# Kernel tuning notes

Measured on AMD Instinct MI355X. Metric: run time of the kernel, lower is better.

Reference implementation:

```python
import jax, jax.numpy as jnp
import numpy as np

S = 1024      # MAX_SEQ_LEN
D_IN = 4096
H = 32        # num_heads
G = 8         # num_kv_groups
HD = 128      # head_dim
GS = H // G   # group_size


def _rope(t, cos, sin):
    # t: [heads, S, HD]; cos/sin: [S, HD]
    half = HD // 2
    t1, t2 = t[..., :half], t[..., half:]
    rotated = jnp.concatenate([-t2, t1], axis=-1)
    return t * cos[None] + rotated * sin[None]


def setup_inputs() -> dict:
    key = jax.random.key(0)
    ks = jax.random.split(key, 8)
    x = jax.random.normal(ks[0], (1, S, D_IN), dtype=jnp.float32)
    mask = jnp.triu(jnp.ones((S, S), dtype=bool), k=1)  # causal: True above diagonal
    # RoPE tables (standard llama frequencies)
    inv_freq = 1.0 / (10000.0 ** (jnp.arange(0, HD, 2, dtype=jnp.float32) / HD))
    angles = jnp.arange(S, dtype=jnp.float32)[:, None] * inv_freq[None, :]  # [S, HD/2]
    angles = jnp.concatenate([angles, angles], axis=-1)                     # [S, HD]
    cos, sin = jnp.cos(angles), jnp.sin(angles)
    sc = 0.02
    Wq = jax.random.normal(ks[1], (D_IN, H * HD), dtype=jnp.float32) * sc
    Wk = jax.random.normal(ks[2], (D_IN, G * HD), dtype=jnp.float32) * sc
    Wv = jax.random.normal(ks[3], (D_IN, G * HD), dtype=jnp.float32) * sc
    Wo = jax.random.normal(ks[4], (H * HD, D_IN), dtype=jnp.float32) * sc
    return {"x": x, "mask": mask, "cos": cos, "sin": sin,
            "Wq": Wq, "Wk": Wk, "Wv": Wv, "Wo": Wo}


def reference(x, mask, cos, sin, Wq, Wk, Wv, Wo):
    b, n_tok, _ = x.shape  # b == 1 (module squeezes dim 0)
    xs = x[0]                                        # [S, d_in]
    q = (xs @ Wq).reshape(n_tok, H, HD).transpose(1, 0, 2)   # [H, S, HD]
    k = (xs @ Wk).reshape(n_tok, G, HD).transpose(1, 0, 2)   # [G, S, HD]
    v = (xs @ Wv).reshape(n_tok, G, HD).transpose(1, 0, 2)   # [G, S, HD]
    q = _rope(q, cos, sin)
    k = _rope(k, cos, sin)
    # GQA expansion: repeat_interleave over head dim
    k = jnp.repeat(k, GS, axis=0)                    # [H, S, HD]
    v = jnp.repeat(v, GS, axis=0)
    scores = jnp.einsum('hsd,htd->hst', q, k)        # [H, S, S]
    scores = jnp.where(mask[None], -jnp.inf, scores) / jnp.sqrt(jnp.float32(HD))
    weights = jax.nn.softmax(scores, axis=-1)
    ctx = jnp.einsum('hst,htd->hsd', weights, v)     # [H, S, HD]
    ctx = ctx.transpose(1, 0, 2).reshape(n_tok, H * HD)
    out = ctx @ Wo                                   # [S, d_in]
    return out[None]                                 # [1, S, d_in]
```

## Files before the change

### kernel.cpp

```cpp
#include <hip/hip_runtime.h>
#include <hip/hip_bf16.h>

#define S_LEN 1024
#define DIN 4096
#define NH 32
#define NG 8
#define HD 128

typedef __bf16 bf16x8 __attribute__((ext_vector_type(8)));
typedef __bf16 bf16x4 __attribute__((ext_vector_type(4)));
typedef float f32x4 __attribute__((ext_vector_type(4)));

__device__ __forceinline__ void gload_lds16(const void* g, void* l) {
  __builtin_amdgcn_global_load_lds(
      (const __attribute__((address_space(1))) unsigned int*)g,
      (__attribute__((address_space(3))) unsigned int*)l, 16, 0, 0);
}

__device__ __forceinline__ unsigned pack2bf(float a, float b) {
  union { __bf16 h[2]; unsigned u; } x;
  x.h[0] = (__bf16)a; x.h[1] = (__bf16)b;
  return x.u;
}

__global__ __launch_bounds__(256) void k_cast(const float* __restrict__ in,
                                              __bf16* __restrict__ out, int n4) {
  int i = blockIdx.x * 256 + threadIdx.x;
  if (i >= n4) return;
  const float4 v = ((const float4*)in)[i];
  bf16x4 o;
  o.x = (__bf16)v.x; o.y = (__bf16)v.y; o.z = (__bf16)v.z; o.w = (__bf16)v.w;
  ((bf16x4*)out)[i] = o;
}

__global__ __launch_bounds__(256) void k_rope(__bf16* __restrict__ Q, __bf16* __restrict__ Kb,
                                              const float* __restrict__ cosT,
                                              const float* __restrict__ sinT) {
  int idx = blockIdx.x * 256 + threadIdx.x;
  int d = (idx & 15) * 4;
  int row = idx >> 4;
  __bf16* p; int s;
  if (row < S_LEN * NH) { p = Q + (size_t)row * HD; s = row >> 5; }
  else { int r = row - S_LEN * NH; p = Kb + (size_t)r * HD; s = r >> 3; }
  const float4 c = *(const float4*)&cosT[s * HD + d];
  const float4 sn = *(const float4*)&sinT[s * HD + d];
  bf16x4 a = *(const bf16x4*)&p[d];
  bf16x4 b = *(const bf16x4*)&p[d + 64];
  bf16x4 oa, ob;
  oa.x = (__bf16)((float)a.x * c.x - (float)b.x * sn.x);
  oa.y = (__bf16)((float)a.y * c.y - (float)b.y * sn.y);
  oa.z = (__bf16)((float)a.z * c.z - (float)b.z * sn.z);
  oa.w = (__bf16)((float)a.w * c.w - (float)b.w * sn.w);
  ob.x = (__bf16)((float)b.x * c.x + (float)a.x * sn.x);
  ob.y = (__bf16)((float)b.y * c.y + (float)a.y * sn.y);
  ob.z = (__bf16)((float)b.z * c.z + (float)a.z * sn.z);
  ob.w = (__bf16)((float)b.w * c.w + (float)a.w * sn.w);
  *(bf16x4*)&p[d] = oa;
  *(bf16x4*)&p[d + 64] = ob;
}

template <int MODE>
__global__ __launch_bounds__(256, 3) void k_gemm(const __bf16* __restrict__ A,
                                                 const float* __restrict__ W0,
                                                 const float* __restrict__ W1,
                                                 const float* __restrict__ W2,
                                                 float* __restrict__ C,
                                                 __bf16* __restrict__ Qb,
                                                 __bf16* __restrict__ Kb,
                                                 __bf16* __restrict__ Vt) {
  __shared__ __bf16 As[2][128 * 64];
  __shared__ unsigned Bp[2][32 * 64];
  const int bm = blockIdx.y, bn = blockIdx.x;
  const int K = DIN, NT = K / 64;

  const float* Wsrc; int ldb, nloc;
  if (MODE == 0) { Wsrc = W0; ldb = 4096; nloc = bn * 64; }
  else {
    if (bn < 64)      { Wsrc = W0; ldb = 4096; nloc = bn * 64; }
    else if (bn < 80) { Wsrc = W1; ldb = 1024; nloc = (bn - 64) * 64; }
    else              { Wsrc = W2; ldb = 1024; nloc = (bn - 80) * 64; }
  }

  const int tid = threadIdx.x, w = tid >> 6;
  const int l = tid & 63, l15 = l & 15, g4 = l >> 4;

  const __bf16* Asrc = A + (size_t)(bm * 128) * K;

  f32x4 acc[2][4];
#pragma unroll
  for (int i = 0; i < 2; ++i)
#pragma unroll
    for (int j = 0; j < 4; ++j)
#pragma unroll
      for (int r = 0; r < 4; ++r) acc[i][j][r] = 0.f;

  float4 breg[2][2];
  const int kp_s[2] = {tid >> 4, 16 + (tid >> 4)};
  const int nn_s = (tid & 15) * 4;

  auto loadB = [&](int t) {
#pragma unroll
    for (int p = 0; p < 2; ++p) {
      const float* src = Wsrc + (size_t)(t * 64 + 2 * kp_s[p]) * ldb + nloc + nn_s;
      breg[p][0] = *(const float4*)src;
      breg[p][1] = *(const float4*)(src + ldb);
    }
  };
  auto writeB = [&](unsigned* dst) {
#pragma unroll
    for (int p = 0; p < 2; ++p) {
      int kp = kp_s[p];
      int cphys = (nn_s >> 2) ^ (kp & 7);
      uint4 d;
      d.x = pack2bf(breg[p][0].x, breg[p][1].x);
      d.y = pack2bf(breg[p][0].y, breg[p][1].y);
      d.z = pack2bf(breg[p][0].z, breg[p][1].z);
      d.w = pack2bf(breg[p][0].w, breg[p][1].w);
      *(uint4*)&dst[kp * 64 + cphys * 4] = d;
    }
  };
  auto issueA = [&](int t, __bf16* dst) {
#pragma unroll
    for (int p = 0; p < 4; ++p) {
      int c = p * 256 + tid;
      int row = c >> 3, gc = (c & 7) ^ (row & 7);
      gload_lds16(Asrc + (size_t)row * K + t * 64 + gc * 8, dst + (p * 256 + w * 64) * 8);
    }
  };
  auto compute = [&](const __bf16* Ab, const unsigned* Bp_) {
    bf16x8 af[2][2];
#pragma unroll
    for (int i = 0; i < 2; ++i) {
      int m = w * 32 + i * 16 + l15;
#pragma unroll
      for (int kk = 0; kk < 2; ++kk)
        af[i][kk] = *(const bf16x8*)((const char*)Ab + m * 128 + (((kk * 4 + g4) ^ (m & 7)) << 4));
    }
    unsigned fbu[2][4][4];
#pragma unroll
    for (int kk = 0; kk < 2; ++kk)
#pragma unroll
      for (int j = 0; j < 4; ++j) {
        int n = j * 16 + l15;
#pragma unroll
        for (int d = 0; d < 4; ++d) {
          int kp = kk * 16 + g4 * 4 + d;
          fbu[kk][j][d] = Bp_[kp * 64 + (((n >> 2) ^ (kp & 7)) << 2) + (n & 3)];
        }
      }
#pragma unroll
    for (int kk = 0; kk < 2; ++kk)
#pragma unroll
      for (int j = 0; j < 4; ++j) {
        union { unsigned u[4]; bf16x8 v; } fb;
        fb.u[0] = fbu[kk][j][0]; fb.u[1] = fbu[kk][j][1];
        fb.u[2] = fbu[kk][j][2]; fb.u[3] = fbu[kk][j][3];
#pragma unroll
        for (int i = 0; i < 2; ++i)
          acc[i][j] = __builtin_amdgcn_mfma_f32_16x16x32_bf16(af[i][kk], fb.v, acc[i][j], 0, 0, 0);
      }
  };

  loadB(0);
  issueA(0, As[0]);
  writeB(Bp[0]);
  __syncthreads();

  for (int t = 0; t < NT; t += 2) {
    loadB(t + 1);
    issueA(t + 1, As[1]);
    compute(As[0], Bp[0]);
    writeB(Bp[1]);
    __syncthreads();
    if (t + 2 < NT) {
      loadB(t + 2);
      issueA(t + 2, As[0]);
    }
    compute(As[1], Bp[1]);
    if (t + 2 < NT) writeB(Bp[0]);
    __syncthreads();
  }

  if constexpr (MODE == 0) {
#pragma unroll
    for (int i = 0; i < 2; ++i)
#pragma unroll
      for (int j = 0; j < 4; ++j)
#pragma unroll
        for (int r = 0; r < 4; ++r) {
          size_t row = bm * 128 + w * 32 + i * 16 + g4 * 4 + r;
          size_t col = bn * 64 + j * 16 + l15;
          C[row * 4096 + col] = acc[i][j][r];
        }
  } else {
    if (bn < 80) {
      __bf16* dst = (bn < 64) ? Qb : Kb;
      int ldc = (bn < 64) ? 4096 : 1024;
#pragma unroll
      for (int i = 0; i < 2; ++i)
#pragma unroll
        for (int j = 0; j < 4; ++j)
#pragma unroll
          for (int r = 0; r < 4; ++r) {
            size_t row = bm * 128 + w * 32 + i * 16 + g4 * 4 + r;
            size_t col = (size_t)nloc + j * 16 + l15;
            dst[row * ldc + col] = (__bf16)acc[i][j][r];
          }
    } else {
#pragma unroll
      for (int i = 0; i < 2; ++i)
#pragma unroll
        for (int j = 0; j < 4; ++j) {
          size_t n = (size_t)nloc + j * 16 + l15;
          size_t m0 = bm * 128 + w * 32 + i * 16 + g4 * 4;
          bf16x4 v;
          v.x = (__bf16)acc[i][j][0]; v.y = (__bf16)acc[i][j][1];
          v.z = (__bf16)acc[i][j][2]; v.w = (__bf16)acc[i][j][3];
          *(bf16x4*)&Vt[n * 1024 + m0] = v;
        }
    }
  }
}

__global__ __launch_bounds__(256) void k_attn(const __bf16* __restrict__ Q,
                                              const __bf16* __restrict__ Kb,
                                              const __bf16* __restrict__ Vt,
                                              __bf16* __restrict__ ctx) {
  __shared__ __align__(16) char lds_raw[65536];
  __bf16* Ks = (__bf16*)lds_raw;
  __bf16* Vs = (__bf16*)(lds_raw + 32768);

  const int h = blockIdx.y, g = h >> 2;
  const int q0 = blockIdx.x * 64;
  const int tid = threadIdx.x, w = tid >> 6, l = tid & 63;
  const int l15 = l & 15, g4 = l >> 4;
  const float scale = 0.08838834764831845f;

  bf16x8 qf[4];
  const int qrow = q0 + w * 16 + l15;
#pragma unroll
  for (int ks = 0; ks < 4; ++ks)
    qf[ks] = *(const bf16x8*)&Q[(size_t)qrow * (NH * HD) + h * HD + ks * 32 + g4 * 8];

  f32x4 acc[8];
#pragma unroll
  for (int i = 0; i < 8; ++i)
#pragma unroll
    for (int r = 0; r < 4; ++r) acc[i][r] = 0.f;
  float m_run = -__builtin_inff(), l_run = 0.f;

  const int ntiles = (q0 + 64 + 127) >> 7;
  for (int kt = 0; kt < ntiles; ++kt) {
    const int kv0 = kt * 128;
#pragma unroll
    for (int p = 0; p < 8; ++p) {
      int c = p * 256 + tid;
      int row = c >> 4, cc = c & 15;
      gload_lds16(&Kb[(size_t)(kv0 + row) * (NG * HD) + g * HD + ((cc ^ (row & 7)) << 3)],
                  &Ks[(p * 256 + w * 64) * 8]);
      gload_lds16(&Vt[(size_t)(g * HD + row) * S_LEN + kv0 + ((cc ^ (row & 7)) << 3)],
                  &Vs[(p * 256 + w * 64) * 8]);
    }
    __syncthreads();

    float sreg[8][4];
    const bool need_mask = (kv0 + 127 > q0);
#pragma unroll
    for (int tf = 0; tf < 8; ++tf) {
      f32x4 sa;
#pragma unroll
      for (int r = 0; r < 4; ++r) sa[r] = 0.f;
      int t_loc = tf * 16 + l15;
#pragma unroll
      for (int ks = 0; ks < 4; ++ks) {
        bf16x8 kf = *(const bf16x8*)((const char*)Ks + t_loc * 256 + (((ks * 4 + g4) ^ (t_loc & 7)) << 4));
        sa = __builtin_amdgcn_mfma_f32_16x16x32_bf16(kf, qf[ks], sa, 0, 0, 0);
      }
#pragma unroll
      for (int r = 0; r < 4; ++r) {
        float v = sa[r] * scale;
        if (need_mask && (kv0 + tf * 16 + g4 * 4 + r) > qrow) v = -__builtin_inff();
        sreg[tf][r] = v;
      }
    }
    float mx = -__builtin_inff();
#pragma unroll
    for (int tf = 0; tf < 8; ++tf)
#pragma unroll
      for (int r = 0; r < 4; ++r) mx = fmaxf(mx, sreg[tf][r]);
    mx = fmaxf(mx, __shfl_xor(mx, 16));
    mx = fmaxf(mx, __shfl_xor(mx, 32));
    const float m_new = fmaxf(m_run, mx);
    const float alpha = __expf(m_run - m_new);
    float ssum = 0.f;
#pragma unroll
    for (int tf = 0; tf < 8; ++tf)
#pragma unroll
      for (int r = 0; r < 4; ++r) {
        sreg[tf][r] = __expf(sreg[tf][r] - m_new);
        ssum += sreg[tf][r];
      }
    ssum += __shfl_xor(ssum, 16);
    ssum += __shfl_xor(ssum, 32);
    l_run = l_run * alpha + ssum;
    m_run = m_new;
    float ar[4];
#pragma unroll
    for (int r = 0; r < 4; ++r) ar[r] = __shfl(alpha, g4 * 4 + r);
#pragma unroll
    for (int nf = 0; nf < 8; ++nf)
#pragma unroll
      for (int r = 0; r < 4; ++r) acc[nf][r] *= ar[r];

    __syncthreads();

    char* pb = lds_raw + w * 4096;
#pragma unroll
    for (int tf = 0; tf < 8; ++tf) {
      int chunkc = 2 * tf + (g4 >> 1);
      int addr = l15 * 256 + ((chunkc ^ (l15 & 7)) << 4) + ((g4 & 1) << 3);
      *(unsigned*)(pb + addr)     = pack2bf(sreg[tf][0], sreg[tf][1]);
      *(unsigned*)(pb + addr + 4) = pack2bf(sreg[tf][2], sreg[tf][3]);
    }
    asm volatile("s_waitcnt lgkmcnt(0)" ::: "memory");
    bf16x8 pf[4];
#pragma unroll
    for (int ks = 0; ks < 4; ++ks)
      pf[ks] = *(const bf16x8*)(pb + l15 * 256 + (((ks * 4 + g4) ^ (l15 & 7)) << 4));
#pragma unroll
    for (int nf = 0; nf < 8; ++nf) {
      int d_loc = nf * 16 + l15;
#pragma unroll
      for (int ks = 0; ks < 4; ++ks) {
        bf16x8 vf = *(const bf16x8*)((const char*)Vs + d_loc * 256 + (((ks * 4 + g4) ^ (d_loc & 7)) << 4));
        acc[nf] = __builtin_amdgcn_mfma_f32_16x16x32_bf16(pf[ks], vf, acc[nf], 0, 0, 0);
      }
    }
    __syncthreads();
  }
  float li[4];
#pragma unroll
  for (int r = 0; r < 4; ++r) li[r] = 1.f / __shfl(l_run, g4 * 4 + r);
#pragma unroll
  for (int nf = 0; nf < 8; ++nf)
#pragma unroll
    for (int r = 0; r < 4; ++r) {
      size_t row = q0 + w * 16 + g4 * 4 + r;
      size_t col = (size_t)h * HD + nf * 16 + l15;
      ctx[row * (NH * HD) + col] = (__bf16)(acc[nf][r] * li[r]);
    }
}

extern "C" void kernel_launch(void* const* d_in, const int* in_sizes, int n_in,
                              void* d_out, int out_size, void* d_ws, size_t ws_size,
                              hipStream_t stream) {
  const float* x    = (const float*)d_in[0];
  const float* cosT = (const float*)d_in[2];
  const float* sinT = (const float*)d_in[3];
  const float* Wq   = (const float*)d_in[4];
  const float* Wk   = (const float*)d_in[5];
  const float* Wv   = (const float*)d_in[6];
  const float* Wo   = (const float*)d_in[7];
  float* out = (float*)d_out;

  char* ws = (char*)d_ws;
  const size_t MB = 1u << 20;
  __bf16* xb   = (__bf16*)(ws + 0);
  __bf16* Qb   = (__bf16*)(ws + 8 * MB);
  __bf16* Kbuf = (__bf16*)(ws + 16 * MB);
  __bf16* Vtb  = (__bf16*)(ws + 18 * MB);
  __bf16* ctxb = (__bf16*)(ws + 0);

  k_cast<<<4096, 256, 0, stream>>>(x, xb, (S_LEN * DIN) / 4);

  k_gemm<1><<<dim3(96, 8), 256, 0, stream>>>(xb, Wq, Wk, Wv, nullptr, Qb, Kbuf, Vtb);

  k_rope<<<2560, 256, 0, stream>>>(Qb, Kbuf, cosT, sinT);

  k_attn<<<dim3(16, 32), 256, 0, stream>>>(Qb, Kbuf, Vtb, ctxb);

  k_gemm<0><<<dim3(64, 8), 256, 0, stream>>>(ctxb, Wo, nullptr, nullptr, out,
                                             nullptr, nullptr, nullptr);
}
```

Baseline: 201.0 us.

## Enlarge GEMM block tile to 128x128 with 2x2 warp layout

Doubles the N dimension of each GEMM block tile from 64 to 128 and arranges the four warps as a 2x2 grid, each computing a 64x64 sub-tile with 16 MFMA accumulators. This raises the compute per LDS fragment load and halves repeated reads of the activation matrix. In exchange it halves the grid sizes, increases register pressure (launch bounds lowered to 2 blocks per CU), and may leave CUs underutilized with fewer waves.

```diff
diff --git a/kernel.cpp b/kernel.cpp
--- a/kernel.cpp
+++ b/kernel.cpp
@@ -60,7 +60,7 @@
 }
 
 template <int MODE>
-__global__ __launch_bounds__(256, 3) void k_gemm(const __bf16* __restrict__ A,
+__global__ __launch_bounds__(256, 2) void k_gemm(const __bf16* __restrict__ A,
                                                  const float* __restrict__ W0,
                                                  const float* __restrict__ W1,
                                                  const float* __restrict__ W2,
@@ -69,54 +69,56 @@
                                                  __bf16* __restrict__ Kb,
                                                  __bf16* __restrict__ Vt) {
   __shared__ __bf16 As[2][128 * 64];
-  __shared__ unsigned Bp[2][32 * 64];
+  __shared__ unsigned Bp[2][32 * 128];
   const int bm = blockIdx.y, bn = blockIdx.x;
   const int K = DIN, NT = K / 64;
 
   const float* Wsrc; int ldb, nloc;
-  if (MODE == 0) { Wsrc = W0; ldb = 4096; nloc = bn * 64; }
+  if (MODE == 0) { Wsrc = W0; ldb = 4096; nloc = bn * 128; }
   else {
-    if (bn < 64)      { Wsrc = W0; ldb = 4096; nloc = bn * 64; }
-    else if (bn < 80) { Wsrc = W1; ldb = 1024; nloc = (bn - 64) * 64; }
-    else              { Wsrc = W2; ldb = 1024; nloc = (bn - 80) * 64; }
+    if (bn < 32)      { Wsrc = W0; ldb = 4096; nloc = bn * 128; }
+    else if (bn < 40) { Wsrc = W1; ldb = 1024; nloc = (bn - 32) * 128; }
+    else              { Wsrc = W2; ldb = 1024; nloc = (bn - 40) * 128; }
   }
 
   const int tid = threadIdx.x, w = tid >> 6;
+  const int wm = w >> 1, wn = w & 1;
   const int l = tid & 63, l15 = l & 15, g4 = l >> 4;
 
   const __bf16* Asrc = A + (size_t)(bm * 128) * K;
 
-  f32x4 acc[2][4];
-#pragma unroll
-  for (int i = 0; i < 2; ++i)
+  f32x4 acc[4][4];
+#pragma unroll
+  for (int i = 0; i < 4; ++i)
 #pragma unroll
     for (int j = 0; j < 4; ++j)
 #pragma unroll
       for (int r = 0; r < 4; ++r) acc[i][j][r] = 0.f;
 
-  float4 breg[2][2];
-  const int kp_s[2] = {tid >> 4, 16 + (tid >> 4)};
-  const int nn_s = (tid & 15) * 4;
+  float4 breg[4][2];
+  const int kp_base = tid >> 5;
+  const int cg = tid & 31;
 
   auto loadB = [&](int t) {
 #pragma unroll
-    for (int p = 0; p < 2; ++p) {
-      const float* src = Wsrc + (size_t)(t * 64 + 2 * kp_s[p]) * ldb + nloc + nn_s;
+    for (int p = 0; p < 4; ++p) {
+      int kp = p * 8 + kp_base;
+      const float* src = Wsrc + (size_t)(t * 64 + 2 * kp) * ldb + nloc + cg * 4;
       breg[p][0] = *(const float4*)src;
       breg[p][1] = *(const float4*)(src + ldb);
     }
   };
   auto writeB = [&](unsigned* dst) {
 #pragma unroll
-    for (int p = 0; p < 2; ++p) {
-      int kp = kp_s[p];
-      int cphys = (nn_s >> 2) ^ (kp & 7);
+    for (int p = 0; p < 4; ++p) {
+      int kp = p * 8 + kp_base;
+      int cphys = cg ^ (kp & 7);
       uint4 d;
       d.x = pack2bf(breg[p][0].x, breg[p][1].x);
       d.y = pack2bf(breg[p][0].y, breg[p][1].y);
       d.z = pack2bf(breg[p][0].z, breg[p][1].z);
       d.w = pack2bf(breg[p][0].w, breg[p][1].w);
-      *(uint4*)&dst[kp * 64 + cphys * 4] = d;
+      *(uint4*)&dst[kp * 128 + cphys * 4] = d;
     }
   };
   auto issueA = [&](int t, __bf16* dst) {
@@ -128,35 +130,28 @@
     }
   };
   auto compute = [&](const __bf16* Ab, const unsigned* Bp_) {
-    bf16x8 af[2][2];
-#pragma unroll
-    for (int i = 0; i < 2; ++i) {
-      int m = w * 32 + i * 16 + l15;
+    bf16x8 af[4][2];
+#pragma unroll
+    for (int i = 0; i < 4; ++i) {
+      int m = wm * 64 + i * 16 + l15;
 #pragma unroll
       for (int kk = 0; kk < 2; ++kk)
         af[i][kk] = *(const bf16x8*)((const char*)Ab + m * 128 + (((kk * 4 + g4) ^ (m & 7)) << 4));
     }
-    unsigned fbu[2][4][4];
 #pragma unroll
     for (int kk = 0; kk < 2; ++kk)
 #pragma unroll
       for (int j = 0; j < 4; ++j) {
-        int n = j * 16 + l15;
+        int n = wn * 64 + j * 16 + l15;
+        int cc = n >> 2, n3 = n & 3;
+        union { unsigned u[4]; bf16x8 v; } fb;
 #pragma unroll
         for (int d = 0; d < 4; ++d) {
           int kp = kk * 16 + g4 * 4 + d;
-          fbu[kk][j][d] = Bp_[kp * 64 + (((n >> 2) ^ (kp & 7)) << 2) + (n & 3)];
+          fb.u[d] = Bp_[kp * 128 + ((cc ^ (kp & 7)) << 2) + n3];
         }
-      }
-#pragma unroll
-    for (int kk = 0; kk < 2; ++kk)
-#pragma unroll
-      for (int j = 0; j < 4; ++j) {
-        union { unsigned u[4]; bf16x8 v; } fb;
-        fb.u[0] = fbu[kk][j][0]; fb.u[1] = fbu[kk][j][1];
-        fb.u[2] = fbu[kk][j][2]; fb.u[3] = fbu[kk][j][3];
-#pragma unroll
-        for (int i = 0; i < 2; ++i)
+#pragma unroll
+        for (int i = 0; i < 4; ++i)
           acc[i][j] = __builtin_amdgcn_mfma_f32_16x16x32_bf16(af[i][kk], fb.v, acc[i][j], 0, 0, 0);
       }
   };
@@ -183,36 +178,36 @@
 
   if constexpr (MODE == 0) {
 #pragma unroll
-    for (int i = 0; i < 2; ++i)
+    for (int i = 0; i < 4; ++i)
 #pragma unroll
       for (int j = 0; j < 4; ++j)
 #pragma unroll
         for (int r = 0; r < 4; ++r) {
-          size_t row = bm * 128 + w * 32 + i * 16 + g4 * 4 + r;
-          size_t col = bn * 64 + j * 16 + l15;
+          size_t row = bm * 128 + wm * 64 + i * 16 + g4 * 4 + r;
+          size_t col = bn * 128 + wn * 64 + j * 16 + l15;
           C[row * 4096 + col] = acc[i][j][r];
         }
   } else {
-    if (bn < 80) {
-      __bf16* dst = (bn < 64) ? Qb : Kb;
-      int ldc = (bn < 64) ? 4096 : 1024;
-#pragma unroll
-      for (int i = 0; i < 2; ++i)
+    if (bn < 40) {
+      __bf16* dst = (bn < 32) ? Qb : Kb;
+      int ldc = (bn < 32) ? 4096 : 1024;
+#pragma unroll
+      for (int i = 0; i < 4; ++i)
 #pragma unroll
         for (int j = 0; j < 4; ++j)
 #pragma unroll
           for (int r = 0; r < 4; ++r) {
-            size_t row = bm * 128 + w * 32 + i * 16 + g4 * 4 + r;
-            size_t col = (size_t)nloc + j * 16 + l15;
+            size_t row = bm * 128 + wm * 64 + i * 16 + g4 * 4 + r;
+            size_t col = (size_t)nloc + wn * 64 + j * 16 + l15;
             dst[row * ldc + col] = (__bf16)acc[i][j][r];
           }
     } else {
 #pragma unroll
-      for (int i = 0; i < 2; ++i)
+      for (int i = 0; i < 4; ++i)
 #pragma unroll
         for (int j = 0; j < 4; ++j) {
-          size_t n = (size_t)nloc + j * 16 + l15;
-          size_t m0 = bm * 128 + w * 32 + i * 16 + g4 * 4;
+          size_t n = (size_t)nloc + wn * 64 + j * 16 + l15;
+          size_t m0 = bm * 128 + wm * 64 + i * 16 + g4 * 4;
           bf16x4 v;
           v.x = (__bf16)acc[i][j][0]; v.y = (__bf16)acc[i][j][1];
           v.z = (__bf16)acc[i][j][2]; v.w = (__bf16)acc[i][j][3];
@@ -373,12 +368,12 @@
 
   k_cast<<<4096, 256, 0, stream>>>(x, xb, (S_LEN * DIN) / 4);
 
-  k_gemm<1><<<dim3(96, 8), 256, 0, stream>>>(xb, Wq, Wk, Wv, nullptr, Qb, Kbuf, Vtb);
+  k_gemm<1><<<dim3(48, 8), 256, 0, stream>>>(xb, Wq, Wk, Wv, nullptr, Qb, Kbuf, Vtb);
 
   k_rope<<<2560, 256, 0, stream>>>(Qb, Kbuf, cosT, sinT);
 
   k_attn<<<dim3(16, 32), 256, 0, stream>>>(Qb, Kbuf, Vtb, ctxb);
 
-  k_gemm<0><<<dim3(64, 8), 256, 0, stream>>>(ctxb, Wo, nullptr, nullptr, out,
+  k_gemm<0><<<dim3(32, 8), 256, 0, stream>>>(ctxb, Wo, nullptr, nullptr, out,
                                              nullptr, nullptr, nullptr);
 }
```

New measurement: 218.4 us. 8.7% more time.
